# Performance work log

Hardware: AMD Instinct MI355X
Metric: run time of the kernel (lower is better)

## Reference

```python
import jax, jax.numpy as jnp
import numpy as np

B, N, E, F, H = 2, 10000, 100000, 512, 512
EPS = 1e-5


def setup_inputs() -> dict:
    key = jax.random.key(0)
    ks = jax.random.split(key, 12)
    s = 0.02
    return {
        "node_features": jax.random.normal(ks[0], (B, N, F), jnp.float32),
        "edge_index": jax.random.randint(ks[1], (B, 2, E), 0, N),
        "num_nodes": N,
        "W1": jax.random.normal(ks[2], (F, H), jnp.float32) * s,
        "b1": jnp.zeros((H,), jnp.float32),
        "g1": jnp.ones((H,), jnp.float32),
        "bb1": jnp.zeros((H,), jnp.float32),
        "W2": jax.random.normal(ks[3], (F, H), jnp.float32) * s,
        "b2": jnp.zeros((H,), jnp.float32),
        "g2": jnp.ones((H,), jnp.float32),
        "bb2": jnp.zeros((H,), jnp.float32),
        "W3": jax.random.normal(ks[4], (H, 1), jnp.float32) * s,
        "b3": jnp.zeros((1,), jnp.float32),
        "W4": jax.random.normal(ks[5], (1, 1), jnp.float32) * s,
        "b4": jnp.zeros((1,), jnp.float32),
    }


def _ln(x, g, b):
    mu = jnp.mean(x, axis=-1, keepdims=True)
    var = jnp.var(x, axis=-1, keepdims=True)
    return (x - mu) * jax.lax.rsqrt(var + EPS) * g + b


def _segment_softmax(v, seg, n):
    # stable per-segment softmax over edges (v: [E], seg: [E])
    m = jax.ops.segment_max(v, seg, num_segments=n)
    e = jnp.exp(v - m[seg])
    s = jax.ops.segment_sum(e, seg, num_segments=n)
    return e / s[seg]


def reference(node_features, edge_index, num_nodes, W1, b1, g1, bb1, W2, b2, g2, bb2, W3, b3, W4, b4):
    src = edge_index[:, 0]  # [B, E]
    dst = edge_index[:, 1]  # [B, E]
    Ui = jnp.take_along_axis(node_features, src[..., None], axis=1)  # [B, E, F]
    Uj = jnp.take_along_axis(node_features, dst[..., None], axis=1)  # [B, E, F]
    a1i = _ln(Ui @ W1 + b1, g1, bb1)
    a2j = _ln(Uj @ W2 + b2, g2, bb2)
    a1j = _ln(Uj @ W1 + b1, g1, bb1)
    a2i = _ln(Ui @ W2 + b2, g2, bb2)
    Zij = jax.nn.relu(a1i + a2j) @ W3 + b3  # [B, E, 1]
    Zji = jax.nn.relu(a1j + a2i) @ W3 + b3  # [B, E, 1]
    d = Zij - Zji
    w4 = W4[0, 0]
    Vij = jax.nn.relu(d * w4 + b4)[..., 0]   # [B, E]
    Vji = jax.nn.relu(-d * w4 + b4)[..., 0]  # [B, E]
    seg_sm = jax.vmap(_segment_softmax, in_axes=(0, 0, None))
    Vij_norm = seg_sm(Vij, src, num_nodes)
    Vji_norm = seg_sm(Vji, dst, num_nodes)
    return (Vij_norm, Vji_norm)
```

## Files before the change

kernel.cpp:

```cpp
#include <hip/hip_runtime.h>
#include <stdint.h>

#define BB 2
#define NN 10000
#define EE 100000
#define FF 512
#define HH 512
constexpr int M_ROWS = BB * NN;
constexpr int M_PAD  = 20160;
constexpr int BE     = BB * EE;
constexpr int BNN    = BB * NN;

typedef __attribute__((ext_vector_type(8))) short short8;
typedef __attribute__((ext_vector_type(4))) float f32x4;
typedef __attribute__((ext_vector_type(2))) float f32x2;
typedef _Float16 half2v __attribute__((ext_vector_type(2)));

#define AS1 __attribute__((address_space(1)))
#define AS3 __attribute__((address_space(3)))

__device__ __forceinline__ float b2f(unsigned short u) {
    union { unsigned int i; float f; } v; v.i = ((unsigned int)u) << 16; return v.f;
}
__device__ __forceinline__ unsigned short f2b(float f) {
    unsigned int x = __float_as_uint(f);
    x += 0x7fffu + ((x >> 16) & 1u);
    return (unsigned short)(x >> 16);
}
__device__ __forceinline__ unsigned char f2fp8(float v) {
    unsigned int p = __builtin_amdgcn_cvt_pk_fp8_f32(v, v, 0u, false);
    return (unsigned char)(p & 0xffu);
}
__device__ __forceinline__ half2v uint2h2(unsigned int u) {
    union { unsigned int u; half2v h; } v; v.u = u; return v.h;
}

#if __has_builtin(__builtin_amdgcn_cvt_scalef32_pk_f16_fp8)
  #define CVT8H(u, sel) __builtin_amdgcn_cvt_scalef32_pk_f16_fp8((u), 1.0f, (sel))
#else
  #define CVT8H(u, sel) ({ f32x2 _p = __builtin_amdgcn_cvt_pk_f32_fp8((u), (sel)); \
                           (half2v){(_Float16)_p.x, (_Float16)_p.y}; })
#endif

#if __has_builtin(__builtin_amdgcn_fdot2)
  #define FDOT2(a, b, c) __builtin_amdgcn_fdot2((a), (b), (c), false)
#else
  #define FDOT2(a, b, c) ((float)(a).x * (float)(b).x + (float)(a).y * (float)(b).y + (c))
#endif

constexpr int PREP_CX = 5000;
constexpr int PREP_TR = PREP_CX + 512;
constexpr int PREP_CP = PREP_TR + 17;
constexpr int PREP_NB = PREP_CP + 157;
__global__ __launch_bounds__(256) void prep_k(
    const void* __restrict__ Xraw,
    const void* __restrict__ W1, const void* __restrict__ W2,
    const void* b1, const void* g1, const void* bb1,
    const void* b2, const void* g2, const void* bb2,
    const void* W3, const void* W4, const void* b4,
    int* __restrict__ flag, unsigned short* __restrict__ Xb,
    unsigned short* __restrict__ T1, unsigned short* __restrict__ T2,
    unsigned short* __restrict__ P, float* __restrict__ Z)
{
    __shared__ int sflag;
    __shared__ unsigned short t[32][33];
    const int tid = threadIdx.x;
    const int bid = blockIdx.x;

    if (tid < 64) {
        const unsigned short* x = (const unsigned short*)Xraw;
        int good = 0;
#pragma unroll
        for (int j = 0; j < 2; j++) {
            unsigned short u = x[2 * (tid * 2 + j)];
            int e = (u >> 7) & 0xFF;
            if (e >= 100 && e <= 140) good++;
        }
#pragma unroll
        for (int off = 32; off >= 1; off >>= 1) good += __shfl_xor(good, off, 64);
        if (tid == 0) sflag = (good < 96) ? 1 : 0;
    }
    __syncthreads();
    const int isf = sflag;
    if (bid == 0 && tid == 0) *flag = isf;

    if (bid < PREP_CX) {
        if (!isf) return;
        int i = (bid * 256 + tid) * 8;
        if (i >= M_ROWS * 512) return;
        const float4* f = (const float4*)((const float*)Xraw + i);
        float4 a = f[0], b = f[1];
        short8 o;
        o[0] = (short)f2b(a.x); o[1] = (short)f2b(a.y);
        o[2] = (short)f2b(a.z); o[3] = (short)f2b(a.w);
        o[4] = (short)f2b(b.x); o[5] = (short)f2b(b.y);
        o[6] = (short)f2b(b.z); o[7] = (short)f2b(b.w);
        *(short8*)(Xb + i) = o;
        return;
    }
    if (bid < PREP_TR) {
        int b2i = bid - PREP_CX;
        int bx = b2i & 15, by = (b2i >> 4) & 15, bz = b2i >> 8;
        const void*     W = bz ? W2 : W1;
        unsigned short* T = bz ? T2 : T1;
        int tx = tid & 31, ty = tid >> 5;
        int n0 = bx * 32, k0 = by * 32;
#pragma unroll
        for (int r = 0; r < 4; r++) {
            int k = k0 + ty + r * 8;
            unsigned short v;
            if (isf) v = f2b(((const float*)W)[k * 512 + n0 + tx]);
            else     v = ((const unsigned short*)W)[k * 512 + n0 + tx];
            t[ty + r * 8][tx] = v;
        }
        __syncthreads();
#pragma unroll
        for (int r = 0; r < 4; r++) {
            int n = n0 + ty + r * 8;
            T[n * 512 + k0 + tx] = t[tx][ty + r * 8];
        }
        return;
    }
    if (bid < PREP_CP) {
        int i = (bid - PREP_TR) * 256 + tid;
        if (i >= 4098) return;
        if (i >= 3586) {
            int j = i - 3586;
            float f;
            if (isf) f = ((const float*)W3)[j];
            else     f = b2f(((const unsigned short*)W3)[j]);
            union { _Float16 h; unsigned short u; } cv;
            cv.h = (_Float16)f;
            P[3600 + j] = cv.u;
            return;
        }
        const void* src; int off;
        if      (i < 512)  { src = b1;  off = i; }
        else if (i < 1024) { src = g1;  off = i - 512; }
        else if (i < 1536) { src = bb1; off = i - 1024; }
        else if (i < 2048) { src = b2;  off = i - 1536; }
        else if (i < 2560) { src = g2;  off = i - 2048; }
        else if (i < 3072) { src = bb2; off = i - 2560; }
        else if (i < 3584) { src = W3;  off = i - 3072; }
        else if (i == 3584){ src = W4;  off = 0; }
        else               { src = b4;  off = 0; }
        unsigned short v;
        if (isf) v = f2b(((const float*)src)[off]);
        else     v = ((const unsigned short*)src)[off];
        P[i] = v;
        return;
    }
    {
        int i = (bid - PREP_CP) * 256 + tid;
        if (i < 2 * BNN) Z[i] = 0.f;
    }
}

__global__ __launch_bounds__(512, 2) void gemm_ln7_k(
    const unsigned short* __restrict__ Xraw,
    const unsigned short* __restrict__ Xb,
    const int* __restrict__ flagp,
    const unsigned short* __restrict__ WT1,
    const unsigned short* __restrict__ WT2,
    const unsigned short* __restrict__ bia1, const unsigned short* __restrict__ gg1, const unsigned short* __restrict__ sh1,
    const unsigned short* __restrict__ bia2, const unsigned short* __restrict__ gg2, const unsigned short* __restrict__ sh2,
    unsigned char* __restrict__ a12)
{
    __shared__ __align__(16) unsigned short S[64512];
    __shared__ float red[160][4][2];

    const int sel = blockIdx.y;
    const unsigned short* WT  = sel ? WT2 : WT1;
    const unsigned short* bia = sel ? bia2 : bia1;
    const unsigned short* gg  = sel ? gg2 : gg1;
    const unsigned short* sh  = sel ? sh2 : sh1;
    const int r0   = blockIdx.x * 160;
    const int tid  = threadIdx.x;
    const int lane = tid & 63;
    const int w    = tid >> 6;
    const int mg   = w >> 2;
    const int ng   = w & 3;
    const int aq   = lane >> 4;
    const int l15  = lane & 15;

    const unsigned short* Xsrc = (*flagp) ? Xb : Xraw;

    AS3 char* S3 = (AS3 char*)S;
    const unsigned sb = (unsigned)(unsigned long long)S3;

    f32x4 acc[5][8];
#pragma unroll
    for (int i = 0; i < 5; i++)
#pragma unroll
        for (int j = 0; j < 8; j++) acc[i][j] = (f32x4){0.f, 0.f, 0.f, 0.f};

    const int a_r1 = tid >> 2;
    const int a_k1 = (tid & 3) ^ ((a_r1 >> 1) & 3);
    int r1c = r0 + a_r1; if (r1c > M_ROWS - 1) r1c = M_ROWS - 1;
    const unsigned short* a_g1 = Xsrc + (size_t)r1c * 512 + a_k1 * 8;
    const int a_r2 = 128 + (tid >> 2);
    const int a_k2 = (tid & 3) ^ ((a_r2 >> 1) & 3);
    int r2c = r0 + a_r2; if (r2c > M_ROWS - 1) r2c = M_ROWS - 1;
    const unsigned short* a_g2 = Xsrc + (size_t)r2c * 512 + a_k2 * 8;
    const int b_n0 = tid >> 2;
    const int b_kc = tid & 3;

    auto stage = [&](int kt) {
        const int jj = kt % 3;
        const int k0 = kt * 32;
        __builtin_amdgcn_global_load_lds((const AS1 void*)(a_g1 + k0),
                                         (AS3 void*)(S3 + jj * 10240 + tid * 16), 16, 0, 0);
        if (tid < 128)
            __builtin_amdgcn_global_load_lds((const AS1 void*)(a_g2 + k0),
                                             (AS3 void*)(S3 + jj * 10240 + (512 + tid) * 16), 16, 0, 0);
#pragma unroll
        for (int u = 0; u < 4; u++) {
            int n   = u * 128 + b_n0;
            int kcs = b_kc ^ ((n >> 1) & 3);
            __builtin_amdgcn_global_load_lds((const AS1 void*)(WT + n * 512 + k0 + kcs * 8),
                                             (AS3 void*)(S3 + 30720 + jj * 32768 + (u * 512 + tid) * 16), 16, 0, 0);
        }
    };

    stage(0);
    stage(1);

    for (int it = 0; it < 16; ++it) {
        if (it < 15) {
            if (w < 2) asm volatile("s_waitcnt vmcnt(6)\n\ts_barrier" ::: "memory");
            else       asm volatile("s_waitcnt vmcnt(5)\n\ts_barrier" ::: "memory");
        } else {
            asm volatile("s_waitcnt vmcnt(0)\n\ts_barrier" ::: "memory");
        }
        if (it + 2 < 16) stage(it + 2);

        const unsigned Ab = sb + (unsigned)((it % 3) * 10240);
        const unsigned Bb = sb + 30720u + (unsigned)((it % 3) * 32768);
        short8 af[5], bf[8];
#pragma unroll
        for (int mt = 0; mt < 5; mt++) {
            int m = mg * 80 + mt * 16 + l15;
            unsigned off = Ab + (unsigned)(m * 64 + (aq ^ ((m >> 1) & 3)) * 16);
            asm volatile("ds_read_b128 %0, %1" : "=v"(af[mt]) : "v"(off));
        }
#pragma unroll
        for (int nt = 0; nt < 8; nt++) {
            int n = ng * 128 + nt * 16 + l15;
            unsigned off = Bb + (unsigned)(n * 64 + (aq ^ ((n >> 1) & 3)) * 16);
            asm volatile("ds_read_b128 %0, %1" : "=v"(bf[nt]) : "v"(off));
        }
        asm volatile("s_waitcnt lgkmcnt(0)"
                     : "+v"(af[0]), "+v"(af[1]), "+v"(af[2]), "+v"(af[3]), "+v"(af[4]),
                       "+v"(bf[0]), "+v"(bf[1]), "+v"(bf[2]), "+v"(bf[3]),
                       "+v"(bf[4]), "+v"(bf[5]), "+v"(bf[6]), "+v"(bf[7]) :: "memory");
#pragma unroll
        for (int nt = 0; nt < 8; nt++)
#pragma unroll
            for (int mt = 0; mt < 5; mt++)
                acc[mt][nt] = __builtin_amdgcn_mfma_f32_16x16x32_bf16(af[mt], bf[nt], acc[mt][nt], 0, 0, 0);
    }

    float bcol[8], gcol[8], shcol[8];
#pragma unroll
    for (int nt = 0; nt < 8; nt++) {
        int col = ng * 128 + nt * 16 + l15;
        bcol[nt]  = b2f(bia[col]);
        gcol[nt]  = b2f(gg[col]);
        shcol[nt] = b2f(sh[col]);
    }
#pragma unroll
    for (int mt = 0; mt < 5; mt++)
#pragma unroll
        for (int nt = 0; nt < 8; nt++)
#pragma unroll
            for (int r = 0; r < 4; r++) acc[mt][nt][r] += bcol[nt];

#pragma unroll
    for (int mt = 0; mt < 5; mt++)
#pragma unroll
        for (int r = 0; r < 4; r++) {
            float s = 0.f, q = 0.f;
#pragma unroll
            for (int nt = 0; nt < 8; nt++) { float x = acc[mt][nt][r]; s += x; q += x * x; }
#pragma unroll
            for (int off = 1; off < 16; off <<= 1) {
                s += __shfl_xor(s, off, 64);
                q += __shfl_xor(q, off, 64);
            }
            if (l15 == 0) {
                int row = mg * 80 + mt * 16 + aq * 4 + r;
                red[row][ng][0] = s;
                red[row][ng][1] = q;
            }
        }
    __syncthreads();

    float mean_[5][4], rstd_[5][4];
#pragma unroll
    for (int mt = 0; mt < 5; mt++)
#pragma unroll
        for (int r = 0; r < 4; r++) {
            int row = mg * 80 + mt * 16 + aq * 4 + r;
            float s = red[row][0][0] + red[row][1][0] + red[row][2][0] + red[row][3][0];
            float q = red[row][0][1] + red[row][1][1] + red[row][2][1] + red[row][3][1];
            float mu  = s * (1.f / 512.f);
            float var = q * (1.f / 512.f) - mu * mu;
            mean_[mt][r] = mu;
            rstd_[mt][r] = rsqrtf(var + 1e-5f);
        }

    unsigned char* ot8 = (unsigned char*)S;
#pragma unroll
    for (int mt = 0; mt < 5; mt++)
#pragma unroll
        for (int nt = 0; nt < 8; nt++)
#pragma unroll
            for (int r = 0; r < 4; r++) {
                int row = mg * 80 + mt * 16 + aq * 4 + r;
                int col = ng * 128 + nt * 16 + l15;
                float v = (acc[mt][nt][r] - mean_[mt][r]) * rstd_[mt][r] * gcol[nt] + shcol[nt];
                ot8[row * 528 + col] = f2fp8(v);
            }
    __syncthreads();

    unsigned char* obase = a12 + sel * 512;
#pragma unroll
    for (int u = 0; u < 10; u++) {
        int ci  = u * 512 + tid;
        int row = ci >> 5, cc = (ci & 31) * 16;
        int gr  = r0 + row;
        if (gr < M_ROWS) {
            uint4 vch = *(const uint4*)(ot8 + row * 528 + cc);
            *(uint4*)(obase + (size_t)gr * 1024 + cc) = vch;
        }
    }
}

__global__ __launch_bounds__(256) void edge_k(
    const unsigned char* __restrict__ a12,
    const int* __restrict__ eidx,
    const unsigned short* __restrict__ W3h,
    const unsigned short* __restrict__ W4,
    const unsigned short* __restrict__ b4p,
    float* __restrict__ Vij, float* __restrict__ Vji,
    float* __restrict__ sumI, float* __restrict__ sumJ)
{
    int wid   = (blockIdx.x * 256 + threadIdx.x) >> 6;
    int lane  = threadIdx.x & 63;
    int which = lane >> 5;
    int l     = lane & 31;
    int e0    = wid * 4 + which * 2;
    int b  = e0 / EE, ei = e0 - b * EE;
    const int* ebase = eidx + b * 2 * EE;
    int srcA = ebase[ei],      srcB = ebase[ei + 1];
    int dstA = ebase[EE + ei], dstB = ebase[EE + ei + 1];
    const unsigned char* nb = a12 + (size_t)(b * NN) * 1024;
    const unsigned char* rsA = nb + (size_t)srcA * 1024;
    const unsigned char* rdA = nb + (size_t)dstA * 1024;
    const unsigned char* rsB = nb + (size_t)srcB * 1024;
    const unsigned char* rdB = nb + (size_t)dstB * 1024;
    int o = l * 16;

    uint4 u1sA = *(const uint4*)(rsA + o);
    uint4 u2sA = *(const uint4*)(rsA + 512 + o);
    uint4 u1dA = *(const uint4*)(rdA + o);
    uint4 u2dA = *(const uint4*)(rdA + 512 + o);
    uint4 u1sB = *(const uint4*)(rsB + o);
    uint4 u2sB = *(const uint4*)(rsB + 512 + o);
    uint4 u1dB = *(const uint4*)(rdB + o);
    uint4 u2dB = *(const uint4*)(rdB + 512 + o);
    uint4 w3a = *(const uint4*)(W3h + l * 16);
    uint4 w3b = *(const uint4*)(W3h + l * 16 + 8);

    const unsigned int W3W[8] = {w3a.x, w3a.y, w3a.z, w3a.w, w3b.x, w3b.y, w3b.z, w3b.w};
    const half2v HZ = {(_Float16)0.f, (_Float16)0.f};

    float zijA = 0.f, zjiA = 0.f, zijB = 0.f, zjiB = 0.f;
#define EDGE_STEP(ZI, ZJ, V1S, V2S, V1D, V2D, WI, C, SEL)            \
    {                                                                \
        half2v wv  = uint2h2(W3W[WI]);                               \
        half2v x1s = CVT8H(V1S.C, SEL);                              \
        half2v x2s = CVT8H(V2S.C, SEL);                              \
        half2v x1d = CVT8H(V1D.C, SEL);                              \
        half2v x2d = CVT8H(V2D.C, SEL);                              \
        half2v pij = __builtin_elementwise_max(x1s + x2d, HZ);       \
        half2v pji = __builtin_elementwise_max(x1d + x2s, HZ);       \
        ZI = FDOT2(pij, wv, ZI);                                     \
        ZJ = FDOT2(pji, wv, ZJ);                                     \
    }
#define EDGE_ALL(ZI, ZJ, V1S, V2S, V1D, V2D)                         \
    EDGE_STEP(ZI, ZJ, V1S, V2S, V1D, V2D, 0, x, false)               \
    EDGE_STEP(ZI, ZJ, V1S, V2S, V1D, V2D, 1, x, true)                \
    EDGE_STEP(ZI, ZJ, V1S, V2S, V1D, V2D, 2, y, false)               \
    EDGE_STEP(ZI, ZJ, V1S, V2S, V1D, V2D, 3, y, true)                \
    EDGE_STEP(ZI, ZJ, V1S, V2S, V1D, V2D, 4, z, false)               \
    EDGE_STEP(ZI, ZJ, V1S, V2S, V1D, V2D, 5, z, true)                \
    EDGE_STEP(ZI, ZJ, V1S, V2S, V1D, V2D, 6, w, false)               \
    EDGE_STEP(ZI, ZJ, V1S, V2S, V1D, V2D, 7, w, true)

    EDGE_ALL(zijA, zjiA, u1sA, u2sA, u1dA, u2dA)
    EDGE_ALL(zijB, zjiB, u1sB, u2sB, u1dB, u2dB)
#undef EDGE_ALL
#undef EDGE_STEP

#pragma unroll
    for (int off = 16; off >= 1; off >>= 1) {
        zijA += __shfl_xor(zijA, off, 64);
        zjiA += __shfl_xor(zjiA, off, 64);
        zijB += __shfl_xor(zijB, off, 64);
        zjiB += __shfl_xor(zjiB, off, 64);
    }
    if (l == 0) {
        float w4f = b2f(W4[0]);
        float b4f = b2f(b4p[0]);
        float dA   = zijA - zjiA;
        float vijA = fmaf(dA, w4f, b4f);  vijA = vijA > 0.f ? vijA : 0.f;
        float vjiA = fmaf(-dA, w4f, b4f); vjiA = vjiA > 0.f ? vjiA : 0.f;
        float dB   = zijB - zjiB;
        float vijB = fmaf(dB, w4f, b4f);  vijB = vijB > 0.f ? vijB : 0.f;
        float vjiB = fmaf(-dB, w4f, b4f); vjiB = vjiB > 0.f ? vjiB : 0.f;
        float eijA = expf(vijA), ejiA = expf(vjiA);
        float eijB = expf(vijB), ejiB = expf(vjiB);
        *(float2*)(Vij + e0) = (float2){eijA, eijB};
        *(float2*)(Vji + e0) = (float2){ejiA, ejiB};
        atomicAdd(sumI + b * NN + srcA, eijA);
        atomicAdd(sumJ + b * NN + dstA, ejiA);
        atomicAdd(sumI + b * NN + srcB, eijB);
        atomicAdd(sumJ + b * NN + dstB, ejiB);
    }
}

__global__ __launch_bounds__(256) void norm_k(
    const float* __restrict__ V, const int* __restrict__ eidx,
    const float* __restrict__ sumI, const float* __restrict__ sumJ,
    const int* __restrict__ flag, void* __restrict__ out)
{
    int i = blockIdx.x * 256 + threadIdx.x;
    if (i >= 2 * BE) return;
    int seg; const float* sm;
    if (i < BE) {
        int b = i / EE, e = i - b * EE;
        seg = b * NN + eidx[b * 2 * EE + e];
        sm = sumI;
    } else {
        int j = i - BE;
        int b = j / EE, e = j - b * EE;
        seg = b * NN + eidx[b * 2 * EE + EE + e];
        sm = sumJ;
    }
    float v = V[i] / sm[seg];
    if (*flag) ((float*)out)[i] = v;
    else       ((unsigned short*)out)[i] = f2b(v);
}

extern "C" void kernel_launch(void* const* d_in, const int* in_sizes, int n_in,
                              void* d_out, int out_size, void* d_ws, size_t ws_size,
                              hipStream_t stream)
{
    (void)in_sizes; (void)n_in; (void)out_size; (void)ws_size;
    const void* X_raw = d_in[0];
    const int*  eix   = (const int*)d_in[1];
    const void* W1    = d_in[3];
    const void* b1    = d_in[4];
    const void* g1    = d_in[5];
    const void* bb1   = d_in[6];
    const void* W2    = d_in[7];
    const void* b2    = d_in[8];
    const void* g2    = d_in[9];
    const void* bb2   = d_in[10];
    const void* W3    = d_in[11];
    const void* W4    = d_in[13];
    const void* b4    = d_in[14];

    char* ws = (char*)d_ws;
    size_t off = 0;
    int* flag = (int*)(ws + off);                        off += 16;
    unsigned char*  a12 = (unsigned char*)(ws + off);    off += (size_t)M_ROWS * 1024;
    unsigned short* Xb  = (unsigned short*)(ws + off);   off += (size_t)M_PAD * 512 * 2;
    unsigned short* T1  = (unsigned short*)(ws + off);   off += (size_t)512 * 512 * 2;
    unsigned short* T2  = (unsigned short*)(ws + off);   off += (size_t)512 * 512 * 2;
    unsigned short* P   = (unsigned short*)(ws + off);   off += 16384;
    float* Vbuf = (float*)(ws + off);                    off += (size_t)2 * BE * 4;
    float* Z    = (float*)(ws + off);                    off += (size_t)2 * BNN * 4;
    float* sumI = Z;
    float* sumJ = Z + BNN;

    prep_k<<<PREP_NB, 256, 0, stream>>>(X_raw, W1, W2, b1, g1, bb1, b2, g2, bb2,
                                        W3, W4, b4, flag, Xb, T1, T2, P, Z);
    gemm_ln7_k<<<dim3(126, 2), 512, 0, stream>>>((const unsigned short*)X_raw, Xb, flag,
                                                 T1, T2,
                                                 P, P + 512, P + 1024,
                                                 P + 1536, P + 2048, P + 2560, a12);
    edge_k<<<BE / 16, 256, 0, stream>>>(a12, eix, P + 3600, P + 3584, P + 3585,
                                        Vbuf, Vbuf + BE, sumI, sumJ);
    norm_k<<<(2 * BE + 255) / 256, 256, 0, stream>>>(Vbuf, eix, sumI, sumJ, flag, (unsigned short*)d_out);
}
```

Measured before the change: 215.4 us.

## Replace async LDS triple-buffering with register-staged double buffering in GEMM

The GEMM main loop no longer uses direct global-to-LDS async loads with a three-stage ring. It now prefetches the next K tile into registers, computes on the current LDS buffer, then writes the registers into the alternate LDS buffer (double buffering). B-fragment reads are split into two halves to lower register pressure. This cuts LDS usage and may ease occupancy, but it adds register staging and exposes more global load latency with only one tile of lookahead.

Measured after the change: 215.0 us. About the same (-0.2%).

```diff
diff --git a/kernel.cpp b/kernel.cpp
--- a/kernel.cpp
+++ b/kernel.cpp
@@ -156,7 +156,7 @@
     }
 }
 
-__global__ __launch_bounds__(512, 2) void gemm_ln7_k(
+__global__ __launch_bounds__(512, 2) void gemm_ln11_k(
     const unsigned short* __restrict__ Xraw,
     const unsigned short* __restrict__ Xb,
     const int* __restrict__ flagp,
@@ -166,7 +166,7 @@
     const unsigned short* __restrict__ bia2, const unsigned short* __restrict__ gg2, const unsigned short* __restrict__ sh2,
     unsigned char* __restrict__ a12)
 {
-    __shared__ __align__(16) unsigned short S[64512];
+    __shared__ __align__(16) unsigned short S[43008];
     __shared__ float red[160][4][2];
 
     const int sel = blockIdx.y;
@@ -187,6 +187,7 @@
 
     AS3 char* S3 = (AS3 char*)S;
     const unsigned sb = (unsigned)(unsigned long long)S3;
+    char* Sb = (char*)S;
 
     f32x4 acc[5][8];
 #pragma unroll
@@ -204,39 +205,47 @@
     const unsigned short* a_g2 = Xsrc + (size_t)r2c * 512 + a_k2 * 8;
     const int b_n0 = tid >> 2;
     const int b_kc = tid & 3;
-
-    auto stage = [&](int kt) {
-        const int jj = kt % 3;
-        const int k0 = kt * 32;
-        __builtin_amdgcn_global_load_lds((const AS1 void*)(a_g1 + k0),
-                                         (AS3 void*)(S3 + jj * 10240 + tid * 16), 16, 0, 0);
-        if (tid < 128)
-            __builtin_amdgcn_global_load_lds((const AS1 void*)(a_g2 + k0),
-                                             (AS3 void*)(S3 + jj * 10240 + (512 + tid) * 16), 16, 0, 0);
-#pragma unroll
-        for (int u = 0; u < 4; u++) {
-            int n   = u * 128 + b_n0;
-            int kcs = b_kc ^ ((n >> 1) & 3);
-            __builtin_amdgcn_global_load_lds((const AS1 void*)(WT + n * 512 + k0 + kcs * 8),
-                                             (AS3 void*)(S3 + 30720 + jj * 32768 + (u * 512 + tid) * 16), 16, 0, 0);
-        }
-    };
-
-    stage(0);
-    stage(1);
+    int bgo0, bgo1, bgo2, bgo3;
+    { int n0_ = 0 * 128 + b_n0; bgo0 = n0_ * 512 + (b_kc ^ ((n0_ >> 1) & 3)) * 8; }
+    { int n1_ = 1 * 128 + b_n0; bgo1 = n1_ * 512 + (b_kc ^ ((n1_ >> 1) & 3)) * 8; }
+    { int n2_ = 2 * 128 + b_n0; bgo2 = n2_ * 512 + (b_kc ^ ((n2_ >> 1) & 3)) * 8; }
+    { int n3_ = 3 * 128 + b_n0; bgo3 = n3_ * 512 + (b_kc ^ ((n3_ >> 1) & 3)) * 8; }
+
+    {
+        short8 aS0 = *(const short8*)(a_g1);
+        short8 aS1 = {};
+        if (tid < 128) aS1 = *(const short8*)(a_g2);
+        short8 bS0 = *(const short8*)(WT + bgo0);
+        short8 bS1 = *(const short8*)(WT + bgo1);
+        short8 bS2 = *(const short8*)(WT + bgo2);
+        short8 bS3 = *(const short8*)(WT + bgo3);
+        *(short8*)(Sb + tid * 16) = aS0;
+        if (tid < 128) *(short8*)(Sb + (512 + tid) * 16) = aS1;
+        char* Bp = Sb + 20480;
+        *(short8*)(Bp + (0 * 512 + tid) * 16) = bS0;
+        *(short8*)(Bp + (1 * 512 + tid) * 16) = bS1;
+        *(short8*)(Bp + (2 * 512 + tid) * 16) = bS2;
+        *(short8*)(Bp + (3 * 512 + tid) * 16) = bS3;
+    }
 
     for (int it = 0; it < 16; ++it) {
-        if (it < 15) {
-            if (w < 2) asm volatile("s_waitcnt vmcnt(6)\n\ts_barrier" ::: "memory");
-            else       asm volatile("s_waitcnt vmcnt(5)\n\ts_barrier" ::: "memory");
-        } else {
-            asm volatile("s_waitcnt vmcnt(0)\n\ts_barrier" ::: "memory");
-        }
-        if (it + 2 < 16) stage(it + 2);
-
-        const unsigned Ab = sb + (unsigned)((it % 3) * 10240);
-        const unsigned Bb = sb + 30720u + (unsigned)((it % 3) * 32768);
-        short8 af[5], bf[8];
+        __syncthreads();
+
+        short8 aS0, aS1, bS0, bS1, bS2, bS3;
+        const bool have = (it + 1 < 16);
+        if (have) {
+            const int k0n = (it + 1) * 32;
+            aS0 = *(const short8*)(a_g1 + k0n);
+            if (tid < 128) aS1 = *(const short8*)(a_g2 + k0n);
+            bS0 = *(const short8*)(WT + bgo0 + k0n);
+            bS1 = *(const short8*)(WT + bgo1 + k0n);
+            bS2 = *(const short8*)(WT + bgo2 + k0n);
+            bS3 = *(const short8*)(WT + bgo3 + k0n);
+        }
+
+        const unsigned Ab = sb + (unsigned)((it & 1) * 10240);
+        const unsigned Bb = sb + 20480u + (unsigned)((it & 1) * 32768);
+        short8 af[5], bf[4];
 #pragma unroll
         for (int mt = 0; mt < 5; mt++) {
             int m = mg * 80 + mt * 16 + l15;
@@ -244,20 +253,43 @@
             asm volatile("ds_read_b128 %0, %1" : "=v"(af[mt]) : "v"(off));
         }
 #pragma unroll
-        for (int nt = 0; nt < 8; nt++) {
+        for (int nt = 0; nt < 4; nt++) {
             int n = ng * 128 + nt * 16 + l15;
             unsigned off = Bb + (unsigned)(n * 64 + (aq ^ ((n >> 1) & 3)) * 16);
             asm volatile("ds_read_b128 %0, %1" : "=v"(bf[nt]) : "v"(off));
         }
         asm volatile("s_waitcnt lgkmcnt(0)"
                      : "+v"(af[0]), "+v"(af[1]), "+v"(af[2]), "+v"(af[3]), "+v"(af[4]),
-                       "+v"(bf[0]), "+v"(bf[1]), "+v"(bf[2]), "+v"(bf[3]),
-                       "+v"(bf[4]), "+v"(bf[5]), "+v"(bf[6]), "+v"(bf[7]) :: "memory");
-#pragma unroll
-        for (int nt = 0; nt < 8; nt++)
+                       "+v"(bf[0]), "+v"(bf[1]), "+v"(bf[2]), "+v"(bf[3]) :: "memory");
+#pragma unroll
+        for (int nt = 0; nt < 4; nt++)
 #pragma unroll
             for (int mt = 0; mt < 5; mt++)
                 acc[mt][nt] = __builtin_amdgcn_mfma_f32_16x16x32_bf16(af[mt], bf[nt], acc[mt][nt], 0, 0, 0);
+#pragma unroll
+        for (int nt = 4; nt < 8; nt++) {
+            int n = ng * 128 + nt * 16 + l15;
+            unsigned off = Bb + (unsigned)(n * 64 + (aq ^ ((n >> 1) & 3)) * 16);
+            asm volatile("ds_read_b128 %0, %1" : "=v"(bf[nt - 4]) : "v"(off));
+        }
+        asm volatile("s_waitcnt lgkmcnt(0)"
+                     : "+v"(bf[0]), "+v"(bf[1]), "+v"(bf[2]), "+v"(bf[3]) :: "memory");
+#pragma unroll
+        for (int nt = 4; nt < 8; nt++)
+#pragma unroll
+            for (int mt = 0; mt < 5; mt++)
+                acc[mt][nt] = __builtin_amdgcn_mfma_f32_16x16x32_bf16(af[mt], bf[nt - 4], acc[mt][nt], 0, 0, 0);
+
+        if (have) {
+            const int jj = (it + 1) & 1;
+            *(short8*)(Sb + jj * 10240 + tid * 16) = aS0;
+            if (tid < 128) *(short8*)(Sb + jj * 10240 + (512 + tid) * 16) = aS1;
+            char* Bp = Sb + 20480 + jj * 32768;
+            *(short8*)(Bp + (0 * 512 + tid) * 16) = bS0;
+            *(short8*)(Bp + (1 * 512 + tid) * 16) = bS1;
+            *(short8*)(Bp + (2 * 512 + tid) * 16) = bS2;
+            *(short8*)(Bp + (3 * 512 + tid) * 16) = bS3;
+        }
     }
 
     float bcol[8], gcol[8], shcol[8];
@@ -487,10 +519,10 @@
 
     prep_k<<<PREP_NB, 256, 0, stream>>>(X_raw, W1, W2, b1, g1, bb1, b2, g2, bb2,
                                         W3, W4, b4, flag, Xb, T1, T2, P, Z);
-    gemm_ln7_k<<<dim3(126, 2), 512, 0, stream>>>((const unsigned short*)X_raw, Xb, flag,
-                                                 T1, T2,
-                                                 P, P + 512, P + 1024,
-                                                 P + 1536, P + 2048, P + 2560, a12);
+    gemm_ln11_k<<<dim3(126, 2), 512, 0, stream>>>((const unsigned short*)X_raw, Xb, flag,
+                                                  T1, T2,
+                                                  P, P + 512, P + 1024,
+                                                  P + 1536, P + 2048, P + 2560, a12);
     edge_k<<<BE / 16, 256, 0, stream>>>(a12, eix, P + 3600, P + 3584, P + 3585,
                                         Vbuf, Vbuf + BE, sumI, sumJ);
     norm_k<<<(2 * BE + 255) / 256, 256, 0, stream>>>(Vbuf, eix, sumI, sumJ, flag, (unsigned short*)d_out);
```

## Load A operand directly from global to registers, double-buffer B with K=64 steps

Applied to the files above, without the earlier changes.

The GEMM+LayerNorm kernel no longer stages the A tile (node features) through LDS. Each wave loads its MFMA A fragments directly from global memory into registers. The B (weight) tile is staged in LDS with double buffering at 64-wide K steps instead of triple buffering at 32-wide steps, which halves the number of barriers. This removes LDS traffic and ds_reads for A. In exchange, A global loads are exposed with a full vmcnt(0) wait each iteration, and each wave reads A redundantly across the 4 N-groups.

Result: slower. 227.8 us (+5.8%).

```diff
diff --git a/kernel.cpp b/kernel.cpp
--- a/kernel.cpp
+++ b/kernel.cpp
@@ -156,7 +156,7 @@
     }
 }
 
-__global__ __launch_bounds__(512, 2) void gemm_ln7_k(
+__global__ __launch_bounds__(512, 2) void gemm_ln13_k(
     const unsigned short* __restrict__ Xraw,
     const unsigned short* __restrict__ Xb,
     const int* __restrict__ flagp,
@@ -166,7 +166,7 @@
     const unsigned short* __restrict__ bia2, const unsigned short* __restrict__ gg2, const unsigned short* __restrict__ sh2,
     unsigned char* __restrict__ a12)
 {
-    __shared__ __align__(16) unsigned short S[64512];
+    __shared__ __align__(16) unsigned short S[65536];
     __shared__ float red[160][4][2];
 
     const int sel = blockIdx.y;
@@ -194,70 +194,77 @@
 #pragma unroll
         for (int j = 0; j < 8; j++) acc[i][j] = (f32x4){0.f, 0.f, 0.f, 0.f};
 
-    const int a_r1 = tid >> 2;
-    const int a_k1 = (tid & 3) ^ ((a_r1 >> 1) & 3);
-    int r1c = r0 + a_r1; if (r1c > M_ROWS - 1) r1c = M_ROWS - 1;
-    const unsigned short* a_g1 = Xsrc + (size_t)r1c * 512 + a_k1 * 8;
-    const int a_r2 = 128 + (tid >> 2);
-    const int a_k2 = (tid & 3) ^ ((a_r2 >> 1) & 3);
-    int r2c = r0 + a_r2; if (r2c > M_ROWS - 1) r2c = M_ROWS - 1;
-    const unsigned short* a_g2 = Xsrc + (size_t)r2c * 512 + a_k2 * 8;
+    const unsigned short* a_gm[5];
+#pragma unroll
+    for (int mt = 0; mt < 5; mt++) {
+        int row = r0 + mg * 80 + mt * 16 + l15;
+        if (row > M_ROWS - 1) row = M_ROWS - 1;
+        a_gm[mt] = Xsrc + (size_t)row * 512 + aq * 8;
+    }
+
     const int b_n0 = tid >> 2;
     const int b_kc = tid & 3;
-
-    auto stage = [&](int kt) {
-        const int jj = kt % 3;
-        const int k0 = kt * 32;
-        __builtin_amdgcn_global_load_lds((const AS1 void*)(a_g1 + k0),
-                                         (AS3 void*)(S3 + jj * 10240 + tid * 16), 16, 0, 0);
-        if (tid < 128)
-            __builtin_amdgcn_global_load_lds((const AS1 void*)(a_g2 + k0),
-                                             (AS3 void*)(S3 + jj * 10240 + (512 + tid) * 16), 16, 0, 0);
-#pragma unroll
-        for (int u = 0; u < 4; u++) {
-            int n   = u * 128 + b_n0;
-            int kcs = b_kc ^ ((n >> 1) & 3);
-            __builtin_amdgcn_global_load_lds((const AS1 void*)(WT + n * 512 + k0 + kcs * 8),
-                                             (AS3 void*)(S3 + 30720 + jj * 32768 + (u * 512 + tid) * 16), 16, 0, 0);
-        }
+    auto stageB = [&](int it2) {
+        const int jj = it2 & 1;
+        const int k0 = it2 * 64;
+#pragma unroll
+        for (int h = 0; h < 2; h++)
+#pragma unroll
+            for (int u = 0; u < 4; u++) {
+                int n   = u * 128 + b_n0;
+                int kcs = b_kc ^ ((n >> 1) & 3);
+                __builtin_amdgcn_global_load_lds(
+                    (const AS1 void*)(WT + n * 512 + k0 + h * 32 + kcs * 8),
+                    (AS3 void*)(S3 + jj * 65536 + h * 32768 + (u * 512 + tid) * 16), 16, 0, 0);
+            }
     };
 
-    stage(0);
-    stage(1);
-
-    for (int it = 0; it < 16; ++it) {
-        if (it < 15) {
-            if (w < 2) asm volatile("s_waitcnt vmcnt(6)\n\ts_barrier" ::: "memory");
-            else       asm volatile("s_waitcnt vmcnt(5)\n\ts_barrier" ::: "memory");
-        } else {
-            asm volatile("s_waitcnt vmcnt(0)\n\ts_barrier" ::: "memory");
-        }
-        if (it + 2 < 16) stage(it + 2);
-
-        const unsigned Ab = sb + (unsigned)((it % 3) * 10240);
-        const unsigned Bb = sb + 30720u + (unsigned)((it % 3) * 32768);
-        short8 af[5], bf[8];
-#pragma unroll
-        for (int mt = 0; mt < 5; mt++) {
-            int m = mg * 80 + mt * 16 + l15;
-            unsigned off = Ab + (unsigned)(m * 64 + (aq ^ ((m >> 1) & 3)) * 16);
-            asm volatile("ds_read_b128 %0, %1" : "=v"(af[mt]) : "v"(off));
-        }
-#pragma unroll
-        for (int nt = 0; nt < 8; nt++) {
-            int n = ng * 128 + nt * 16 + l15;
-            unsigned off = Bb + (unsigned)(n * 64 + (aq ^ ((n >> 1) & 3)) * 16);
-            asm volatile("ds_read_b128 %0, %1" : "=v"(bf[nt]) : "v"(off));
-        }
-        asm volatile("s_waitcnt lgkmcnt(0)"
-                     : "+v"(af[0]), "+v"(af[1]), "+v"(af[2]), "+v"(af[3]), "+v"(af[4]),
-                       "+v"(bf[0]), "+v"(bf[1]), "+v"(bf[2]), "+v"(bf[3]),
-                       "+v"(bf[4]), "+v"(bf[5]), "+v"(bf[6]), "+v"(bf[7]) :: "memory");
-#pragma unroll
-        for (int nt = 0; nt < 8; nt++)
+    stageB(0);
+
+    for (int it = 0; it < 8; ++it) {
+        asm volatile("s_waitcnt vmcnt(0)\n\ts_barrier" ::: "memory");
+
+        short8 af[2][5];
+#pragma unroll
+        for (int kc = 0; kc < 2; kc++)
 #pragma unroll
             for (int mt = 0; mt < 5; mt++)
-                acc[mt][nt] = __builtin_amdgcn_mfma_f32_16x16x32_bf16(af[mt], bf[nt], acc[mt][nt], 0, 0, 0);
+                af[kc][mt] = *(const short8*)(a_gm[mt] + it * 64 + kc * 32);
+        __builtin_amdgcn_sched_barrier(0);
+
+        if (it + 1 < 8) stageB(it + 1);
+
+        const unsigned Bb = sb + (unsigned)((it & 1) * 65536);
+#pragma unroll
+        for (int kc = 0; kc < 2; kc++) {
+            short8 bf[4];
+#pragma unroll
+            for (int nt = 0; nt < 4; nt++) {
+                int n = ng * 128 + nt * 16 + l15;
+                unsigned off = Bb + (unsigned)(kc * 32768 + n * 64 + (aq ^ ((n >> 1) & 3)) * 16);
+                asm volatile("ds_read_b128 %0, %1" : "=v"(bf[nt]) : "v"(off));
+            }
+            asm volatile("s_waitcnt lgkmcnt(0)"
+                         : "+v"(bf[0]), "+v"(bf[1]), "+v"(bf[2]), "+v"(bf[3]) :: "memory");
+#pragma unroll
+            for (int nt = 0; nt < 4; nt++)
+#pragma unroll
+                for (int mt = 0; mt < 5; mt++)
+                    acc[mt][nt] = __builtin_amdgcn_mfma_f32_16x16x32_bf16(af[kc][mt], bf[nt], acc[mt][nt], 0, 0, 0);
+#pragma unroll
+            for (int nt = 4; nt < 8; nt++) {
+                int n = ng * 128 + nt * 16 + l15;
+                unsigned off = Bb + (unsigned)(kc * 32768 + n * 64 + (aq ^ ((n >> 1) & 3)) * 16);
+                asm volatile("ds_read_b128 %0, %1" : "=v"(bf[nt - 4]) : "v"(off));
+            }
+            asm volatile("s_waitcnt lgkmcnt(0)"
+                         : "+v"(bf[0]), "+v"(bf[1]), "+v"(bf[2]), "+v"(bf[3]) :: "memory");
+#pragma unroll
+            for (int nt = 4; nt < 8; nt++)
+#pragma unroll
+                for (int mt = 0; mt < 5; mt++)
+                    acc[mt][nt] = __builtin_amdgcn_mfma_f32_16x16x32_bf16(af[kc][mt], bf[nt - 4], acc[mt][nt], 0, 0, 0);
+        }
     }
 
     float bcol[8], gcol[8], shcol[8];
@@ -487,10 +494,10 @@
 
     prep_k<<<PREP_NB, 256, 0, stream>>>(X_raw, W1, W2, b1, g1, bb1, b2, g2, bb2,
                                         W3, W4, b4, flag, Xb, T1, T2, P, Z);
-    gemm_ln7_k<<<dim3(126, 2), 512, 0, stream>>>((const unsigned short*)X_raw, Xb, flag,
-                                                 T1, T2,
-                                                 P, P + 512, P + 1024,
-                                                 P + 1536, P + 2048, P + 2560, a12);
+    gemm_ln13_k<<<dim3(126, 2), 512, 0, stream>>>((const unsigned short*)X_raw, Xb, flag,
+                                                  T1, T2,
+                                                  P, P + 512, P + 1024,
+                                                  P + 1536, P + 2048, P + 2560, a12);
     edge_k<<<BE / 16, 256, 0, stream>>>(a12, eix, P + 3600, P + 3584, P + 3585,
                                         Vbuf, Vbuf + BE, sumI, sumJ);
     norm_k<<<(2 * BE + 255) / 256, 256, 0, stream>>>(Vbuf, eix, sumI, sumJ, flag, (unsigned short*)d_out);
```
